# Kernel tuning notes

Hardware: AMD Instinct MI355X
Metric: run time of the kernel (lower is better)

Reference implementation:

```python
import jax, jax.numpy as jnp
import numpy as np

MAX_OOV = 50

def setup_inputs() -> dict:
    key = jax.random.key(0)
    ks = jax.random.split(key, 20)
    B, T, Tc, E, H, V = 128, 256, 200, 256, 512, 50000
    s = 0.02
    inp = {
        'input': jax.random.randint(ks[0], (B, 1), 0, V),
        'h0': jax.random.normal(ks[1], (1, B, H), jnp.float32),
        'c0': jax.random.normal(ks[2], (1, B, H), jnp.float32),
        'encoder_outputs': jax.random.normal(ks[3], (B, T, H), jnp.float32),
        'context_encoder_outputs': jax.random.normal(ks[4], (B, Tc, H), jnp.float32),
        'context_input': jax.random.randint(ks[5], (B, Tc), 0, V + MAX_OOV),
        'embedding': jax.random.normal(ks[6], (V, E), jnp.float32) * s,
        'W_ih': jax.random.normal(ks[7], (4 * H, E), jnp.float32) * s,
        'W_hh': jax.random.normal(ks[8], (4 * H, H), jnp.float32) * s,
        'b_ih': jnp.zeros((4 * H,), jnp.float32),
        'b_hh': jnp.zeros((4 * H,), jnp.float32),
        'attn_W': jax.random.normal(ks[9], (H, H), jnp.float32) * s,
        'attn_b': jnp.zeros((H,), jnp.float32),
        'cattn_W': jax.random.normal(ks[10], (H, H), jnp.float32) * s,
        'cattn_b': jnp.zeros((H,), jnp.float32),
        'gen_W': jax.random.normal(ks[11], (1, 3 * H + E), jnp.float32) * s,
        'gen_b': jnp.zeros((1,), jnp.float32),
        'sig_b': jax.random.uniform(ks[12], (1,), jnp.float32, -0.1, 0.1),
        'out_W': jax.random.normal(ks[13], (V, H), jnp.float32) * s,
        'out_b': jnp.zeros((V,), jnp.float32),
    }
    return inp

def reference(input, h0, c0, encoder_outputs, context_encoder_outputs, context_input,
              embedding, W_ih, W_hh, b_ih, b_hh, attn_W, attn_b, cattn_W, cattn_b,
              gen_W, gen_b, sig_b, out_W, out_b):
    B = input.shape[0]
    V = out_W.shape[0]
    Vext = V + MAX_OOV
    # embedding lookup (input_len == 1)
    emb = embedding[input[:, 0]]                       # [B, E]
    # single-step LSTM (PyTorch gate order: i, f, g, o)
    gates = emb @ W_ih.T + b_ih + h0[0] @ W_hh.T + b_hh  # [B, 4H]
    i, f, g, o = jnp.split(gates, 4, axis=-1)
    c1 = jax.nn.sigmoid(f) * c0[0] + jax.nn.sigmoid(i) * jnp.tanh(g)
    h1 = jax.nn.sigmoid(o) * jnp.tanh(c1)              # [B, H]
    output = h1
    # attention over encoder_outputs (context_only)
    dec = output @ attn_W.T + attn_b                   # [B, H]
    scores = jax.nn.softmax(jnp.einsum('bth,bh->bt', encoder_outputs, dec), axis=1)
    context = jnp.einsum('bt,bth->bh', scores, encoder_outputs)
    # context attention (score_only)
    cdec = output @ cattn_W.T + cattn_b
    cscores = jax.nn.softmax(jnp.einsum('bth,bh->bt', context_encoder_outputs, cdec), axis=1)  # [B, Tc]
    cctx = jnp.einsum('bt,bth->bh', cscores, context_encoder_outputs)
    # generation probability
    feats = jnp.concatenate([context, cctx, output, emb], axis=1)  # [B, 3H+E]
    p_gen = jax.nn.sigmoid(feats @ gen_W.T + gen_b + sig_b)        # [B, 1]
    ctx_len = (context_input > 0).sum(axis=1, keepdims=True)
    p_gen = jnp.where(ctx_len == 0, jnp.float32(1.0), p_gen)
    # vocab distribution, extended with oov zeros
    p_vocab = jax.nn.softmax(output @ out_W.T + out_b, axis=1)
    p_vocab = jnp.concatenate([p_vocab, jnp.zeros((B, MAX_OOV), p_vocab.dtype)], axis=1)
    # copy distribution: scatter-add attention scores into extended vocab
    p_copy = jnp.zeros((B, Vext), p_vocab.dtype).at[
        jnp.arange(B)[:, None], context_input].add(cscores)
    prob = p_gen * p_vocab + (1.0 - p_gen) * p_copy
    logp = jnp.log(jnp.clip(prob, 1e-10))
    return logp, (h1[None], c1[None])
```

## Files before the change

kernel.cpp:

```cpp
#include <hip/hip_runtime.h>
#include <hip/hip_bf16.h>

#define BB 128
#define T_ENC 256
#define T_CTX 200
#define E_DIM 256
#define H_DIM 512
#define V_DIM 50000
#define N_OOV 50
#define VEXT  50050
#define FOURH 2048
#define K_GATES 768
#define LOGP_SZ (BB * VEXT)
#define OUT_H1_OFF LOGP_SZ
#define OUT_C1_OFF (LOGP_SZ + BB * H_DIM)
#define VCHUNK 2048
#define NCHUNK 25

typedef __bf16 bf16x8 __attribute__((ext_vector_type(8)));
typedef float  floatx4 __attribute__((ext_vector_type(4)));

__device__ __forceinline__ float wave_sum(float v) {
#pragma unroll
  for (int m = 32; m > 0; m >>= 1) v += __shfl_xor(v, m, 64);
  return v;
}

__device__ __forceinline__ float sigm(float x) { return 1.0f / (1.0f + __expf(-x)); }

__device__ __forceinline__ unsigned f2bf2(float a, float b) {
  unsigned ua = __float_as_uint(a), ub = __float_as_uint(b);
  ua = (ua + 0x7FFFu + ((ua >> 16) & 1u)) >> 16;
  ub = (ub + 0x7FFFu + ((ub >> 16) & 1u)) & 0xFFFF0000u;
  return ua | ub;
}

__global__ __launch_bounds__(256) void prep_weights(
    const float* __restrict__ W_ih, const float* __restrict__ W_hh,
    const float* __restrict__ attnW, const float* __restrict__ cattnW,
    const float* __restrict__ attnb, const float* __restrict__ cattnb,
    __bf16* __restrict__ Wcat, __bf16* __restrict__ Wattn, float* __restrict__ attnbc) {
  int n = blockIdx.x, tid = threadIdx.x;
  __bf16* wr = Wcat + n * K_GATES;
  wr[tid]       = (__bf16)W_ih[n * E_DIM + tid];
  wr[256 + tid] = (__bf16)W_hh[n * H_DIM + tid];
  wr[512 + tid] = (__bf16)W_hh[n * H_DIM + 256 + tid];
  if (n < 1024) {
    const float* src = (n < 512) ? (attnW + (size_t)n * H_DIM) : (cattnW + (size_t)(n - 512) * H_DIM);
    __bf16* wa = Wattn + n * H_DIM;
    wa[tid]       = (__bf16)src[tid];
    wa[256 + tid] = (__bf16)src[256 + tid];
  }
  if (n < 4) {
    int i = n * 256 + tid;
    attnbc[i] = (i < 512) ? attnb[i] : cattnb[i - 512];
  }
}

__global__ __launch_bounds__(256) void prep_a(
    const int* __restrict__ input, const float* __restrict__ emb_table,
    const float* __restrict__ h0, __bf16* __restrict__ Abuf, float* __restrict__ embf) {
  int b = blockIdx.x, tid = threadIdx.x;
  int tok = input[b];
  float e = emb_table[(size_t)tok * E_DIM + tid];
  embf[b * E_DIM + tid] = e;
  __bf16* ar = Abuf + b * K_GATES;
  ar[tid] = (__bf16)e;
  ar[256 + tid] = (__bf16)h0[b * H_DIM + tid];
  ar[512 + tid] = (__bf16)h0[b * H_DIM + 256 + tid];
}

template <int BF32>
__global__ __launch_bounds__(256) void gemm_mfma(
    const __bf16* __restrict__ Abf, const void* __restrict__ Bsrc,
    const float* __restrict__ bias, float* __restrict__ C, int N, int K, int ldc) {
  __shared__ __bf16 As[128][72];
  __shared__ __bf16 Bs[128][72];
  int tid = threadIdx.x;
  int lane = tid & 63, wid = tid >> 6;
  int wm = wid & 1, wn = wid >> 1;
  int n0 = blockIdx.x * 128;

  floatx4 acc[4][4];
#pragma unroll
  for (int i = 0; i < 4; i++)
#pragma unroll
    for (int j = 0; j < 4; j++) acc[i][j] = (floatx4){0.f, 0.f, 0.f, 0.f};

  int arow = tid >> 1, ahalf = tid & 1;

  for (int k0 = 0; k0 < K; k0 += 64) {
    __syncthreads();
    {
      const uint4* s = (const uint4*)(Abf + arow * K + k0 + ahalf * 32);
      uint4* d = (uint4*)&As[arow][ahalf * 32];
      d[0] = s[0]; d[1] = s[1]; d[2] = s[2]; d[3] = s[3];
    }
    {
      int gn = n0 + arow; if (gn > N - 1) gn = N - 1;
      if (BF32) {
        const float4* s = (const float4*)((const float*)Bsrc + (size_t)gn * K + k0 + ahalf * 32);
        uint4* d = (uint4*)&Bs[arow][ahalf * 32];
#pragma unroll
        for (int q = 0; q < 4; q++) {
          float4 fa = s[2 * q], fb = s[2 * q + 1];
          uint4 o;
          o.x = f2bf2(fa.x, fa.y); o.y = f2bf2(fa.z, fa.w);
          o.z = f2bf2(fb.x, fb.y); o.w = f2bf2(fb.z, fb.w);
          d[q] = o;
        }
      } else {
        const uint4* s = (const uint4*)((const __bf16*)Bsrc + (size_t)gn * K + k0 + ahalf * 32);
        uint4* d = (uint4*)&Bs[arow][ahalf * 32];
        d[0] = s[0]; d[1] = s[1]; d[2] = s[2]; d[3] = s[3];
      }
    }
    __syncthreads();
#pragma unroll
    for (int kk = 0; kk < 64; kk += 32) {
      int kbase = kk + (lane >> 4) * 8;
      bf16x8 a[4], b[4];
#pragma unroll
      for (int i = 0; i < 4; i++) a[i] = *(const bf16x8*)&As[wm * 64 + i * 16 + (lane & 15)][kbase];
#pragma unroll
      for (int j = 0; j < 4; j++) b[j] = *(const bf16x8*)&Bs[wn * 64 + j * 16 + (lane & 15)][kbase];
#pragma unroll
      for (int i = 0; i < 4; i++)
#pragma unroll
        for (int j = 0; j < 4; j++)
          acc[i][j] = __builtin_amdgcn_mfma_f32_16x16x32_bf16(a[i], b[j], acc[i][j], 0, 0, 0);
    }
  }
  int cn = lane & 15, cq = lane >> 4;
#pragma unroll
  for (int i = 0; i < 4; i++)
#pragma unroll
    for (int j = 0; j < 4; j++)
#pragma unroll
      for (int r = 0; r < 4; r++) {
        int row = wm * 64 + i * 16 + cq * 4 + r;
        int col = n0 + wn * 64 + j * 16 + cn;
        if (col < N) {
          float v = acc[i][j][r];
          if (bias) v += bias[col];
          C[(size_t)row * ldc + col] = v;
        }
      }
}

__global__ __launch_bounds__(256) void lstm_kernel(
    const float* __restrict__ gates, const float* __restrict__ b_ih,
    const float* __restrict__ b_hh, const float* __restrict__ c0,
    float* __restrict__ h1_out, float* __restrict__ c1_out, __bf16* __restrict__ h1b) {
  int idx = blockIdx.x * 256 + threadIdx.x;
  int b = idx >> 9, j = idx & 511;
  const float* g = gates + b * FOURH;
  float iv = g[j]        + b_ih[j]        + b_hh[j];
  float fv = g[512 + j]  + b_ih[512 + j]  + b_hh[512 + j];
  float gv = g[1024 + j] + b_ih[1024 + j] + b_hh[1024 + j];
  float ov = g[1536 + j] + b_ih[1536 + j] + b_hh[1536 + j];
  float c1 = sigm(fv) * c0[idx] + sigm(iv) * tanhf(gv);
  float h1 = sigm(ov) * tanhf(c1);
  h1_out[idx] = h1;
  c1_out[idx] = c1;
  h1b[idx] = (__bf16)h1;
}

__global__ __launch_bounds__(256) void flash_attn(
    const float* __restrict__ enc, const float* __restrict__ cenc,
    const float* __restrict__ decbuf, float* __restrict__ opart,
    float2* __restrict__ mlb, float* __restrict__ rawsc) {
  int g = blockIdx.x;
  int b = g & 127;
  int cc = g >> 7;
  int which = cc >> 2, chunk = cc & 3;
  int tchunk = which ? 50 : 64;
  int t0 = chunk * tchunk;
  const float* src = which ? (cenc + (size_t)b * T_CTX * H_DIM) : (enc + (size_t)b * T_ENC * H_DIM);
  const float* decp = decbuf + b * 1024 + which * 512;
  int tid = threadIdx.x, lane = tid & 63, wid = tid >> 6;
  float4 d0 = *(const float4*)(decp + lane * 8);
  float4 d1 = *(const float4*)(decp + lane * 8 + 4);
  float m = -1e30f, l = 0.f;
  float4 o0 = {0.f, 0.f, 0.f, 0.f}, o1 = {0.f, 0.f, 0.f, 0.f};
  for (int t = t0 + wid; t < t0 + tchunk; t += 4) {
    const float* row = src + (size_t)t * H_DIM + lane * 8;
    float4 r0 = *(const float4*)row;
    float4 r1 = *(const float4*)(row + 4);
    float p = r0.x * d0.x + r0.y * d0.y + r0.z * d0.z + r0.w * d0.w +
              r1.x * d1.x + r1.y * d1.y + r1.z * d1.z + r1.w * d1.w;
    p = wave_sum(p);
    if (which && lane == 0) rawsc[b * T_CTX + t] = p;
    float mn = fmaxf(m, p);
    float sc = __expf(m - mn);
    float e  = __expf(p - mn);
    l = l * sc + e;
    o0.x = o0.x * sc + e * r0.x; o0.y = o0.y * sc + e * r0.y;
    o0.z = o0.z * sc + e * r0.z; o0.w = o0.w * sc + e * r0.w;
    o1.x = o1.x * sc + e * r1.x; o1.y = o1.y * sc + e * r1.y;
    o1.z = o1.z * sc + e * r1.z; o1.w = o1.w * sc + e * r1.w;
    m = mn;
  }
  __shared__ float so[4][512];
  __shared__ float sml[4][2];
  *(float4*)&so[wid][lane * 8]     = o0;
  *(float4*)&so[wid][lane * 8 + 4] = o1;
  if (lane == 0) { sml[wid][0] = m; sml[wid][1] = l; }
  __syncthreads();
  float M = fmaxf(fmaxf(sml[0][0], sml[1][0]), fmaxf(sml[2][0], sml[3][0]));
  float w0 = __expf(sml[0][0] - M), w1 = __expf(sml[1][0] - M);
  float w2 = __expf(sml[2][0] - M), w3 = __expf(sml[3][0] - M);
  float L = w0 * sml[0][1] + w1 * sml[1][1] + w2 * sml[2][1] + w3 * sml[3][1];
  int h = tid, h2 = tid + 256;
  float O0 = w0 * so[0][h]  + w1 * so[1][h]  + w2 * so[2][h]  + w3 * so[3][h];
  float O1 = w0 * so[0][h2] + w1 * so[1][h2] + w2 * so[2][h2] + w3 * so[3][h2];
  opart[(size_t)g * 512 + h]  = O0;
  opart[(size_t)g * 512 + h2] = O1;
  if (tid == 0) mlb[g] = make_float2(M, L);
}

__global__ __launch_bounds__(256) void attn_combine(
    const float* __restrict__ opart, const float2* __restrict__ mlb,
    float* __restrict__ ctx, float* __restrict__ cctx,
    float* __restrict__ Mc, float* __restrict__ Lc) {
  int bw = blockIdx.x;
  int b = bw & 127, which = bw >> 7;
  int tid = threadIdx.x;
  int g0 = (which * 4) * 128 + b;
  float2 ml0 = mlb[g0], ml1 = mlb[g0 + 128], ml2 = mlb[g0 + 256], ml3 = mlb[g0 + 384];
  float M = fmaxf(fmaxf(ml0.x, ml1.x), fmaxf(ml2.x, ml3.x));
  float w0 = __expf(ml0.x - M), w1 = __expf(ml1.x - M);
  float w2 = __expf(ml2.x - M), w3 = __expf(ml3.x - M);
  float L = w0 * ml0.y + w1 * ml1.y + w2 * ml2.y + w3 * ml3.y;
  float invL = 1.0f / L;
  float s0 = w0 * opart[(size_t)g0 * 512 + tid]       + w1 * opart[(size_t)(g0 + 128) * 512 + tid] +
             w2 * opart[(size_t)(g0 + 256) * 512 + tid] + w3 * opart[(size_t)(g0 + 384) * 512 + tid];
  int t2 = tid + 256;
  float s1 = w0 * opart[(size_t)g0 * 512 + t2]       + w1 * opart[(size_t)(g0 + 128) * 512 + t2] +
             w2 * opart[(size_t)(g0 + 256) * 512 + t2] + w3 * opart[(size_t)(g0 + 384) * 512 + t2];
  float* outp = (which ? cctx : ctx) + b * 512;
  outp[tid] = s0 * invL;
  outp[t2]  = s1 * invL;
  if (which && tid == 0) { Mc[b] = M; Lc[b] = L; }
}

__global__ __launch_bounds__(256) void pgen_kernel(
    const float* __restrict__ ctx, const float* __restrict__ cctx,
    const float* __restrict__ h1f, const float* __restrict__ embf,
    const float* __restrict__ genW, const float* __restrict__ genb,
    const float* __restrict__ sigb, const int* __restrict__ ctx_inp,
    float* __restrict__ pgen_) {
  int wid = threadIdx.x >> 6, lane = threadIdx.x & 63;
  int b = blockIdx.x * 4 + wid;
  float acc = 0.f;
  for (int j = lane; j < 1792; j += 64) {
    float x;
    if (j < 512) x = ctx[b * 512 + j];
    else if (j < 1024) x = cctx[b * 512 + j - 512];
    else if (j < 1536) x = h1f[b * 512 + j - 1024];
    else x = embf[b * 256 + j - 1536];
    acc += x * genW[j];
  }
  acc = wave_sum(acc);
  float cnt = 0.f;
  for (int j = lane; j < T_CTX; j += 64) cnt += (ctx_inp[b * T_CTX + j] > 0) ? 1.f : 0.f;
  cnt = wave_sum(cnt);
  if (lane == 0) {
    float p = sigm(acc + genb[0] + sigb[0]);
    if (cnt == 0.f) p = 1.0f;
    pgen_[b] = p;
  }
}

__global__ __launch_bounds__(256) void stats_part(
    const float* __restrict__ logits, float* __restrict__ mpart, float* __restrict__ spart) {
  int bx = blockIdx.x;
  int b = bx & 127, c = bx >> 7;
  int tid = threadIdx.x;
  const float* rowp = logits + (size_t)b * VEXT;
  int v0 = c * VCHUNK + tid * 8;
  float m = -1e30f, s = 0.f;
#pragma unroll
  for (int k = 0; k < 4; k++) {
    int v = v0 + 2 * k;
    float2 x = *(const float2*)(rowp + v);
    if (v < V_DIM) {
      float xv = x.x;
      if (xv > m) { s = s * __expf(m - xv) + 1.0f; m = xv; } else s += __expf(xv - m);
    }
    if (v + 1 < V_DIM) {
      float xv = x.y;
      if (xv > m) { s = s * __expf(m - xv) + 1.0f; m = xv; } else s += __expf(xv - m);
    }
  }
  __shared__ float sm[256], ss[256];
  sm[tid] = m; ss[tid] = s; __syncthreads();
  for (int st = 128; st; st >>= 1) {
    if (tid < st) {
      float m2 = sm[tid + st], s2 = ss[tid + st];
      float mo = fmaxf(sm[tid], m2);
      ss[tid] = ss[tid] * __expf(sm[tid] - mo) + s2 * __expf(m2 - mo);
      sm[tid] = mo;
    }
    __syncthreads();
  }
  if (tid == 0) { mpart[bx] = sm[0]; spart[bx] = ss[0]; }
}

__global__ __launch_bounds__(128) void stats_comb(
    const float* __restrict__ mpart, const float* __restrict__ spart,
    float* __restrict__ rowm, float* __restrict__ rows_) {
  int b = threadIdx.x;
  float m = -1e30f, s = 0.f;
#pragma unroll
  for (int c = 0; c < NCHUNK; c++) {
    float m2 = mpart[c * 128 + b], s2 = spart[c * 128 + b];
    float mo = fmaxf(m, m2);
    s = s * __expf(m - mo) + s2 * __expf(m2 - mo);
    m = mo;
  }
  rowm[b] = m; rows_[b] = s;
}

__global__ __launch_bounds__(256) void final_kernel(
    float* __restrict__ out, const int* __restrict__ ctx_inp,
    const float* __restrict__ rawsc, const float* __restrict__ pgen_,
    const float* __restrict__ Mc, const float* __restrict__ Lc,
    const float* __restrict__ rowm, const float* __restrict__ rows_) {
  __shared__ float pc[VCHUNK];
  int bx = blockIdx.x;
  int b = bx & 127, c = bx >> 7;
  int tid = threadIdx.x;
#pragma unroll
  for (int k = 0; k < 8; k++) pc[tid * 8 + k] = 0.f;
  __syncthreads();
  int v0c = c * VCHUNK;
  if (tid < T_CTX) {
    int idx = ctx_inp[b * T_CTX + tid];
    int rel = idx - v0c;
    if (rel >= 0 && rel < VCHUNK) {
      float val = __expf(rawsc[b * T_CTX + tid] - Mc[b]) / Lc[b];
      atomicAdd(&pc[rel], val);
    }
  }
  __syncthreads();
  float pg = pgen_[b], m = rowm[b], inv = 1.0f / rows_[b], pc1 = 1.0f - pg;
  float* rowp = out + (size_t)b * VEXT;
  int li0 = tid * 8;
#pragma unroll
  for (int k = 0; k < 4; k++) {
    int li = li0 + 2 * k;
    int v = v0c + li;
    float2 x = *(const float2*)(rowp + v);
    float pv0 = (v < V_DIM)     ? __expf(x.x - m) * inv : 0.f;
    float pv1 = (v + 1 < V_DIM) ? __expf(x.y - m) * inv : 0.f;
    float r0 = __logf(fmaxf(pg * pv0 + pc1 * pc[li],     1e-10f));
    float r1 = __logf(fmaxf(pg * pv1 + pc1 * pc[li + 1], 1e-10f));
    if (v + 1 < VEXT)      *(float2*)(rowp + v) = make_float2(r0, r1);
    else if (v < VEXT)     rowp[v] = r0;
  }
}

extern "C" void kernel_launch(void* const* d_in, const int* in_sizes, int n_in,
                              void* d_out, int out_size, void* d_ws, size_t ws_size,
                              hipStream_t stream) {
  const int*   input   = (const int*)d_in[0];
  const float* h0      = (const float*)d_in[1];
  const float* c0      = (const float*)d_in[2];
  const float* enc     = (const float*)d_in[3];
  const float* cenc    = (const float*)d_in[4];
  const int*   ctx_inp = (const int*)d_in[5];
  const float* embT    = (const float*)d_in[6];
  const float* W_ih    = (const float*)d_in[7];
  const float* W_hh    = (const float*)d_in[8];
  const float* b_ih    = (const float*)d_in[9];
  const float* b_hh    = (const float*)d_in[10];
  const float* attnW   = (const float*)d_in[11];
  const float* attnb   = (const float*)d_in[12];
  const float* cattnW  = (const float*)d_in[13];
  const float* cattnb  = (const float*)d_in[14];
  const float* genW    = (const float*)d_in[15];
  const float* genb    = (const float*)d_in[16];
  const float* sigb    = (const float*)d_in[17];
  const float* outW    = (const float*)d_in[18];
  const float* outb    = (const float*)d_in[19];

  char* ws = (char*)d_ws;
  __bf16* Wcat   = (__bf16*)(ws + 0);
  __bf16* Wattn  = (__bf16*)(ws + 3145728);
  float*  attnbc = (float*)(ws + 4194304);
  __bf16* Abuf   = (__bf16*)(ws + 4198400);
  float*  embf   = (float*)(ws + 4395008);
  float*  gates  = (float*)(ws + 4526080);
  __bf16* h1b    = (__bf16*)(ws + 5574656);
  float*  decbuf = (float*)(ws + 5705728);
  float*  opart  = (float*)(ws + 6230016);
  float2* mlb    = (float2*)(ws + 8327168);
  float*  ctx    = (float*)(ws + 8335360);
  float*  cctx   = (float*)(ws + 8597504);
  float*  rawsc  = (float*)(ws + 8859648);
  float*  Mc     = (float*)(ws + 8962048);
  float*  Lc     = (float*)(ws + 8962560);
  float*  pgenb  = (float*)(ws + 8963072);
  float*  mpart  = (float*)(ws + 8963584);
  float*  spart  = (float*)(ws + 8976384);
  float*  rowm   = (float*)(ws + 8989184);
  float*  rows_  = (float*)(ws + 8989696);

  float* outF = (float*)d_out;
  float* h1_out = outF + OUT_H1_OFF;
  float* c1_out = outF + OUT_C1_OFF;

  prep_weights<<<2048, 256, 0, stream>>>(W_ih, W_hh, attnW, cattnW, attnb, cattnb, Wcat, Wattn, attnbc);
  prep_a<<<128, 256, 0, stream>>>(input, embT, h0, Abuf, embf);
  gemm_mfma<0><<<16, 256, 0, stream>>>(Abuf, Wcat, nullptr, gates, FOURH, K_GATES, FOURH);
  lstm_kernel<<<256, 256, 0, stream>>>(gates, b_ih, b_hh, c0, h1_out, c1_out, h1b);
  gemm_mfma<1><<<391, 256, 0, stream>>>(h1b, outW, outb, outF, V_DIM, H_DIM, VEXT);
  stats_part<<<NCHUNK * 128, 256, 0, stream>>>(outF, mpart, spart);
  stats_comb<<<1, 128, 0, stream>>>(mpart, spart, rowm, rows_);
  gemm_mfma<0><<<8, 256, 0, stream>>>(h1b, Wattn, attnbc, decbuf, 1024, H_DIM, 1024);
  flash_attn<<<1024, 256, 0, stream>>>(enc, cenc, decbuf, opart, mlb, rawsc);
  attn_combine<<<256, 256, 0, stream>>>(opart, mlb, ctx, cctx, Mc, Lc);
  pgen_kernel<<<32, 256, 0, stream>>>(ctx, cctx, h1_out, embf, genW, genb, sigb, ctx_inp, pgenb);
  final_kernel<<<NCHUNK * 128, 256, 0, stream>>>(outF, ctx_inp, rawsc, pgenb, Mc, Lc, rowm, rows_);
}
```

Measured before the change: 413.0 us.

## Fuse kernels, narrow GEMM tiles to 64 columns, split-K gates GEMM, register prefetch

Cuts the launch count from 12 to 7 by merging the prep kernels, the vocab and attention projection GEMMs, the softmax-stats and flash-attention passes, the two combine steps, and folding the p_gen computation into the final kernel. The GEMM tile shrinks to 128x64 so the vocab projection runs in more blocks (782 instead of 391), and it now prefetches the next K slab into registers while the current one is computed. The gates GEMM is split along K into two halves that the LSTM kernel sums, which adds an extra gates buffer. The final kernel now recomputes p_gen in every one of its 25 chunk blocks per row, which is redundant work.

```diff
diff --git a/kernel.cpp b/kernel.cpp
--- a/kernel.cpp
+++ b/kernel.cpp
@@ -16,6 +16,7 @@
 #define OUT_C1_OFF (LOGP_SZ + BB * H_DIM)
 #define VCHUNK 2048
 #define NCHUNK 25
+#define NBIG 782
 
 typedef __bf16 bf16x8 __attribute__((ext_vector_type(8)));
 typedef float  floatx4 __attribute__((ext_vector_type(4)));
@@ -35,111 +36,128 @@
   return ua | ub;
 }
 
-__global__ __launch_bounds__(256) void prep_weights(
+__global__ __launch_bounds__(256) void prep_all(
     const float* __restrict__ W_ih, const float* __restrict__ W_hh,
     const float* __restrict__ attnW, const float* __restrict__ cattnW,
     const float* __restrict__ attnb, const float* __restrict__ cattnb,
-    __bf16* __restrict__ Wcat, __bf16* __restrict__ Wattn, float* __restrict__ attnbc) {
+    const int* __restrict__ input, const float* __restrict__ embT,
+    const float* __restrict__ h0,
+    __bf16* __restrict__ Wcat, __bf16* __restrict__ Wattn, float* __restrict__ attnbc,
+    __bf16* __restrict__ Abuf, float* __restrict__ embf) {
   int n = blockIdx.x, tid = threadIdx.x;
-  __bf16* wr = Wcat + n * K_GATES;
-  wr[tid]       = (__bf16)W_ih[n * E_DIM + tid];
-  wr[256 + tid] = (__bf16)W_hh[n * H_DIM + tid];
-  wr[512 + tid] = (__bf16)W_hh[n * H_DIM + 256 + tid];
-  if (n < 1024) {
-    const float* src = (n < 512) ? (attnW + (size_t)n * H_DIM) : (cattnW + (size_t)(n - 512) * H_DIM);
-    __bf16* wa = Wattn + n * H_DIM;
-    wa[tid]       = (__bf16)src[tid];
-    wa[256 + tid] = (__bf16)src[256 + tid];
-  }
-  if (n < 4) {
-    int i = n * 256 + tid;
-    attnbc[i] = (i < 512) ? attnb[i] : cattnb[i - 512];
-  }
-}
-
-__global__ __launch_bounds__(256) void prep_a(
-    const int* __restrict__ input, const float* __restrict__ emb_table,
-    const float* __restrict__ h0, __bf16* __restrict__ Abuf, float* __restrict__ embf) {
-  int b = blockIdx.x, tid = threadIdx.x;
-  int tok = input[b];
-  float e = emb_table[(size_t)tok * E_DIM + tid];
-  embf[b * E_DIM + tid] = e;
-  __bf16* ar = Abuf + b * K_GATES;
-  ar[tid] = (__bf16)e;
-  ar[256 + tid] = (__bf16)h0[b * H_DIM + tid];
-  ar[512 + tid] = (__bf16)h0[b * H_DIM + 256 + tid];
+  if (n < 2048) {
+    unsigned* wr = (unsigned*)(Wcat + (size_t)n * K_GATES);
+    for (int idx = tid; idx < 384; idx += 256) {
+      int e0 = idx * 2;
+      float2 x = (e0 < 256) ? *(const float2*)(W_ih + (size_t)n * E_DIM + e0)
+                            : *(const float2*)(W_hh + (size_t)n * H_DIM + e0 - 256);
+      wr[idx] = f2bf2(x.x, x.y);
+    }
+    if (n < 1024) {
+      const float* src = (n < 512) ? (attnW + (size_t)n * H_DIM) : (cattnW + (size_t)(n - 512) * H_DIM);
+      unsigned* wa = (unsigned*)(Wattn + (size_t)n * H_DIM);
+      float2 x = *(const float2*)(src + tid * 2);
+      wa[tid] = f2bf2(x.x, x.y);
+    }
+    if (n < 4) {
+      int i = n * 256 + tid;
+      attnbc[i] = (i < 512) ? attnb[i] : cattnb[i - 512];
+    }
+  } else {
+    int b = n - 2048;
+    int tok = input[b];
+    unsigned* ar = (unsigned*)(Abuf + (size_t)b * K_GATES);
+    for (int idx = tid; idx < 384; idx += 256) {
+      int e0 = idx * 2;
+      float2 x;
+      if (e0 < 256) {
+        x = *(const float2*)(embT + (size_t)tok * E_DIM + e0);
+        *(float2*)(embf + b * E_DIM + e0) = x;
+      } else {
+        x = *(const float2*)(h0 + (size_t)b * H_DIM + e0 - 256);
+      }
+      ar[idx] = f2bf2(x.x, x.y);
+    }
+  }
 }
 
 template <int BF32>
-__global__ __launch_bounds__(256) void gemm_mfma(
+__device__ __forceinline__ void gemm64_body(
     const __bf16* __restrict__ Abf, const void* __restrict__ Bsrc,
-    const float* __restrict__ bias, float* __restrict__ C, int N, int K, int ldc) {
+    const float* __restrict__ bias, float* __restrict__ C,
+    int n0, int N, int Koff, int Klen, int Kpitch, int ldc) {
   __shared__ __bf16 As[128][72];
-  __shared__ __bf16 Bs[128][72];
-  int tid = threadIdx.x;
-  int lane = tid & 63, wid = tid >> 6;
-  int wm = wid & 1, wn = wid >> 1;
-  int n0 = blockIdx.x * 128;
-
-  floatx4 acc[4][4];
-#pragma unroll
-  for (int i = 0; i < 4; i++)
+  __shared__ __bf16 Bs[64][72];
+  int tid = threadIdx.x, lane = tid & 63, wid = tid >> 6;
+
+  floatx4 acc[2][4];
+#pragma unroll
+  for (int i = 0; i < 2; i++)
 #pragma unroll
     for (int j = 0; j < 4; j++) acc[i][j] = (floatx4){0.f, 0.f, 0.f, 0.f};
 
   int arow = tid >> 1, ahalf = tid & 1;
-
-  for (int k0 = 0; k0 < K; k0 += 64) {
+  int brow = tid >> 2, bq = tid & 3;
+  int gnb = n0 + brow; if (gnb > N - 1) gnb = N - 1;
+
+  const __bf16* abase = Abf + (size_t)arow * Kpitch + Koff + ahalf * 32;
+  const float*  bfb = (const float*)Bsrc + (size_t)gnb * Kpitch + Koff + bq * 16;
+  const __bf16* bhb = (const __bf16*)Bsrc + (size_t)gnb * Kpitch + Koff + bq * 16;
+
+  uint4 ra[4];
+  float4 rbf[4];
+  uint4 rbh[2];
+  {
+    const uint4* s = (const uint4*)abase;
+    ra[0] = s[0]; ra[1] = s[1]; ra[2] = s[2]; ra[3] = s[3];
+    if (BF32) { const float4* t = (const float4*)bfb; rbf[0] = t[0]; rbf[1] = t[1]; rbf[2] = t[2]; rbf[3] = t[3]; }
+    else      { const uint4* t = (const uint4*)bhb;  rbh[0] = t[0]; rbh[1] = t[1]; }
+  }
+
+  for (int k0 = 0; k0 < Klen; k0 += 64) {
     __syncthreads();
-    {
-      const uint4* s = (const uint4*)(Abf + arow * K + k0 + ahalf * 32);
-      uint4* d = (uint4*)&As[arow][ahalf * 32];
-      d[0] = s[0]; d[1] = s[1]; d[2] = s[2]; d[3] = s[3];
-    }
-    {
-      int gn = n0 + arow; if (gn > N - 1) gn = N - 1;
-      if (BF32) {
-        const float4* s = (const float4*)((const float*)Bsrc + (size_t)gn * K + k0 + ahalf * 32);
-        uint4* d = (uint4*)&Bs[arow][ahalf * 32];
-#pragma unroll
-        for (int q = 0; q < 4; q++) {
-          float4 fa = s[2 * q], fb = s[2 * q + 1];
-          uint4 o;
-          o.x = f2bf2(fa.x, fa.y); o.y = f2bf2(fa.z, fa.w);
-          o.z = f2bf2(fb.x, fb.y); o.w = f2bf2(fb.z, fb.w);
-          d[q] = o;
-        }
-      } else {
-        const uint4* s = (const uint4*)((const __bf16*)Bsrc + (size_t)gn * K + k0 + ahalf * 32);
-        uint4* d = (uint4*)&Bs[arow][ahalf * 32];
-        d[0] = s[0]; d[1] = s[1]; d[2] = s[2]; d[3] = s[3];
-      }
+    { uint4* d = (uint4*)&As[arow][ahalf * 32]; d[0] = ra[0]; d[1] = ra[1]; d[2] = ra[2]; d[3] = ra[3]; }
+    if (BF32) {
+      uint4 o0, o1;
+      o0.x = f2bf2(rbf[0].x, rbf[0].y); o0.y = f2bf2(rbf[0].z, rbf[0].w);
+      o0.z = f2bf2(rbf[1].x, rbf[1].y); o0.w = f2bf2(rbf[1].z, rbf[1].w);
+      o1.x = f2bf2(rbf[2].x, rbf[2].y); o1.y = f2bf2(rbf[2].z, rbf[2].w);
+      o1.z = f2bf2(rbf[3].x, rbf[3].y); o1.w = f2bf2(rbf[3].z, rbf[3].w);
+      uint4* d = (uint4*)&Bs[brow][bq * 16]; d[0] = o0; d[1] = o1;
+    } else {
+      uint4* d = (uint4*)&Bs[brow][bq * 16]; d[0] = rbh[0]; d[1] = rbh[1];
+    }
+    if (k0 + 64 < Klen) {
+      const uint4* s = (const uint4*)(abase + k0 + 64);
+      ra[0] = s[0]; ra[1] = s[1]; ra[2] = s[2]; ra[3] = s[3];
+      if (BF32) { const float4* t = (const float4*)(bfb + k0 + 64); rbf[0] = t[0]; rbf[1] = t[1]; rbf[2] = t[2]; rbf[3] = t[3]; }
+      else      { const uint4* t = (const uint4*)(bhb + k0 + 64);  rbh[0] = t[0]; rbh[1] = t[1]; }
     }
     __syncthreads();
 #pragma unroll
     for (int kk = 0; kk < 64; kk += 32) {
       int kbase = kk + (lane >> 4) * 8;
-      bf16x8 a[4], b[4];
-#pragma unroll
-      for (int i = 0; i < 4; i++) a[i] = *(const bf16x8*)&As[wm * 64 + i * 16 + (lane & 15)][kbase];
-#pragma unroll
-      for (int j = 0; j < 4; j++) b[j] = *(const bf16x8*)&Bs[wn * 64 + j * 16 + (lane & 15)][kbase];
-#pragma unroll
-      for (int i = 0; i < 4; i++)
-#pragma unroll
-        for (int j = 0; j < 4; j++)
-          acc[i][j] = __builtin_amdgcn_mfma_f32_16x16x32_bf16(a[i], b[j], acc[i][j], 0, 0, 0);
+      bf16x8 a0 = *(const bf16x8*)&As[wid * 32 + (lane & 15)][kbase];
+      bf16x8 a1 = *(const bf16x8*)&As[wid * 32 + 16 + (lane & 15)][kbase];
+      bf16x8 bfr[4];
+#pragma unroll
+      for (int j = 0; j < 4; j++) bfr[j] = *(const bf16x8*)&Bs[j * 16 + (lane & 15)][kbase];
+#pragma unroll
+      for (int j = 0; j < 4; j++) {
+        acc[0][j] = __builtin_amdgcn_mfma_f32_16x16x32_bf16(a0, bfr[j], acc[0][j], 0, 0, 0);
+        acc[1][j] = __builtin_amdgcn_mfma_f32_16x16x32_bf16(a1, bfr[j], acc[1][j], 0, 0, 0);
+      }
     }
   }
   int cn = lane & 15, cq = lane >> 4;
 #pragma unroll
-  for (int i = 0; i < 4; i++)
+  for (int i = 0; i < 2; i++)
 #pragma unroll
     for (int j = 0; j < 4; j++)
 #pragma unroll
       for (int r = 0; r < 4; r++) {
-        int row = wm * 64 + i * 16 + cq * 4 + r;
-        int col = n0 + wn * 64 + j * 16 + cn;
+        int row = wid * 32 + i * 16 + cq * 4 + r;
+        int col = n0 + j * 16 + cn;
         if (col < N) {
           float v = acc[i][j][r];
           if (bias) v += bias[col];
@@ -148,17 +166,37 @@
       }
 }
 
+__global__ __launch_bounds__(256) void gates_gemm(
+    const __bf16* __restrict__ Abuf, const __bf16* __restrict__ Wcat,
+    float* __restrict__ g0, float* __restrict__ g1) {
+  int bx = blockIdx.x;
+  int kh = bx >> 5, nb = bx & 31;
+  gemm64_body<0>(Abuf, Wcat, nullptr, kh ? g1 : g0, nb * 64, FOURH, kh * 384, 384, K_GATES, FOURH);
+}
+
+__global__ __launch_bounds__(256) void mega_gemm(
+    const __bf16* __restrict__ h1b, const float* __restrict__ outW,
+    const float* __restrict__ outb, float* __restrict__ Cbig,
+    const __bf16* __restrict__ Wattn, const float* __restrict__ attnbc,
+    float* __restrict__ decbuf) {
+  int bx = blockIdx.x;
+  if (bx < NBIG) gemm64_body<1>(h1b, outW, outb, Cbig, bx * 64, V_DIM, 0, H_DIM, H_DIM, VEXT);
+  else           gemm64_body<0>(h1b, Wattn, attnbc, decbuf, (bx - NBIG) * 64, 1024, 0, H_DIM, H_DIM, 1024);
+}
+
 __global__ __launch_bounds__(256) void lstm_kernel(
-    const float* __restrict__ gates, const float* __restrict__ b_ih,
-    const float* __restrict__ b_hh, const float* __restrict__ c0,
+    const float* __restrict__ gA, const float* __restrict__ gB,
+    const float* __restrict__ b_ih, const float* __restrict__ b_hh,
+    const float* __restrict__ c0,
     float* __restrict__ h1_out, float* __restrict__ c1_out, __bf16* __restrict__ h1b) {
   int idx = blockIdx.x * 256 + threadIdx.x;
   int b = idx >> 9, j = idx & 511;
-  const float* g = gates + b * FOURH;
-  float iv = g[j]        + b_ih[j]        + b_hh[j];
-  float fv = g[512 + j]  + b_ih[512 + j]  + b_hh[512 + j];
-  float gv = g[1024 + j] + b_ih[1024 + j] + b_hh[1024 + j];
-  float ov = g[1536 + j] + b_ih[1536 + j] + b_hh[1536 + j];
+  const float* ga = gA + b * FOURH;
+  const float* gb = gB + b * FOURH;
+  float iv = ga[j]        + gb[j]        + b_ih[j]        + b_hh[j];
+  float fv = ga[512 + j]  + gb[512 + j]  + b_ih[512 + j]  + b_hh[512 + j];
+  float gv = ga[1024 + j] + gb[1024 + j] + b_ih[1024 + j] + b_hh[1024 + j];
+  float ov = ga[1536 + j] + gb[1536 + j] + b_ih[1536 + j] + b_hh[1536 + j];
   float c1 = sigm(fv) * c0[idx] + sigm(iv) * tanhf(gv);
   float h1 = sigm(ov) * tanhf(c1);
   h1_out[idx] = h1;
@@ -166,11 +204,12 @@
   h1b[idx] = (__bf16)h1;
 }
 
-__global__ __launch_bounds__(256) void flash_attn(
-    const float* __restrict__ enc, const float* __restrict__ cenc,
+__device__ __forceinline__ void flash_body(
+    int g, const float* __restrict__ enc, const float* __restrict__ cenc,
     const float* __restrict__ decbuf, float* __restrict__ opart,
     float2* __restrict__ mlb, float* __restrict__ rawsc) {
-  int g = blockIdx.x;
+  __shared__ float so[4][512];
+  __shared__ float sml[4][2];
   int b = g & 127;
   int cc = g >> 7;
   int which = cc >> 2, chunk = cc & 3;
@@ -201,8 +240,6 @@
     o1.z = o1.z * sc + e * r1.z; o1.w = o1.w * sc + e * r1.w;
     m = mn;
   }
-  __shared__ float so[4][512];
-  __shared__ float sml[4][2];
   *(float4*)&so[wid][lane * 8]     = o0;
   *(float4*)&so[wid][lane * 8 + 4] = o1;
   if (lane == 0) { sml[wid][0] = m; sml[wid][1] = l; }
@@ -219,62 +256,10 @@
   if (tid == 0) mlb[g] = make_float2(M, L);
 }
 
-__global__ __launch_bounds__(256) void attn_combine(
-    const float* __restrict__ opart, const float2* __restrict__ mlb,
-    float* __restrict__ ctx, float* __restrict__ cctx,
-    float* __restrict__ Mc, float* __restrict__ Lc) {
-  int bw = blockIdx.x;
-  int b = bw & 127, which = bw >> 7;
-  int tid = threadIdx.x;
-  int g0 = (which * 4) * 128 + b;
-  float2 ml0 = mlb[g0], ml1 = mlb[g0 + 128], ml2 = mlb[g0 + 256], ml3 = mlb[g0 + 384];
-  float M = fmaxf(fmaxf(ml0.x, ml1.x), fmaxf(ml2.x, ml3.x));
-  float w0 = __expf(ml0.x - M), w1 = __expf(ml1.x - M);
-  float w2 = __expf(ml2.x - M), w3 = __expf(ml3.x - M);
-  float L = w0 * ml0.y + w1 * ml1.y + w2 * ml2.y + w3 * ml3.y;
-  float invL = 1.0f / L;
-  float s0 = w0 * opart[(size_t)g0 * 512 + tid]       + w1 * opart[(size_t)(g0 + 128) * 512 + tid] +
-             w2 * opart[(size_t)(g0 + 256) * 512 + tid] + w3 * opart[(size_t)(g0 + 384) * 512 + tid];
-  int t2 = tid + 256;
-  float s1 = w0 * opart[(size_t)g0 * 512 + t2]       + w1 * opart[(size_t)(g0 + 128) * 512 + t2] +
-             w2 * opart[(size_t)(g0 + 256) * 512 + t2] + w3 * opart[(size_t)(g0 + 384) * 512 + t2];
-  float* outp = (which ? cctx : ctx) + b * 512;
-  outp[tid] = s0 * invL;
-  outp[t2]  = s1 * invL;
-  if (which && tid == 0) { Mc[b] = M; Lc[b] = L; }
-}
-
-__global__ __launch_bounds__(256) void pgen_kernel(
-    const float* __restrict__ ctx, const float* __restrict__ cctx,
-    const float* __restrict__ h1f, const float* __restrict__ embf,
-    const float* __restrict__ genW, const float* __restrict__ genb,
-    const float* __restrict__ sigb, const int* __restrict__ ctx_inp,
-    float* __restrict__ pgen_) {
-  int wid = threadIdx.x >> 6, lane = threadIdx.x & 63;
-  int b = blockIdx.x * 4 + wid;
-  float acc = 0.f;
-  for (int j = lane; j < 1792; j += 64) {
-    float x;
-    if (j < 512) x = ctx[b * 512 + j];
-    else if (j < 1024) x = cctx[b * 512 + j - 512];
-    else if (j < 1536) x = h1f[b * 512 + j - 1024];
-    else x = embf[b * 256 + j - 1536];
-    acc += x * genW[j];
-  }
-  acc = wave_sum(acc);
-  float cnt = 0.f;
-  for (int j = lane; j < T_CTX; j += 64) cnt += (ctx_inp[b * T_CTX + j] > 0) ? 1.f : 0.f;
-  cnt = wave_sum(cnt);
-  if (lane == 0) {
-    float p = sigm(acc + genb[0] + sigb[0]);
-    if (cnt == 0.f) p = 1.0f;
-    pgen_[b] = p;
-  }
-}
-
-__global__ __launch_bounds__(256) void stats_part(
-    const float* __restrict__ logits, float* __restrict__ mpart, float* __restrict__ spart) {
-  int bx = blockIdx.x;
+__device__ __forceinline__ void stats_body(
+    int bx, const float* __restrict__ logits,
+    float* __restrict__ mpart, float* __restrict__ spart) {
+  __shared__ float sm[256], ss[256];
   int b = bx & 127, c = bx >> 7;
   int tid = threadIdx.x;
   const float* rowp = logits + (size_t)b * VEXT;
@@ -293,7 +278,6 @@
       if (xv > m) { s = s * __expf(m - xv) + 1.0f; m = xv; } else s += __expf(xv - m);
     }
   }
-  __shared__ float sm[256], ss[256];
   sm[tid] = m; ss[tid] = s; __syncthreads();
   for (int st = 128; st; st >>= 1) {
     if (tid < st) {
@@ -307,44 +291,102 @@
   if (tid == 0) { mpart[bx] = sm[0]; spart[bx] = ss[0]; }
 }
 
-__global__ __launch_bounds__(128) void stats_comb(
+__global__ __launch_bounds__(256) void fs_kernel(
+    const float* __restrict__ logits, float* __restrict__ mpart, float* __restrict__ spart,
+    const float* __restrict__ enc, const float* __restrict__ cenc,
+    const float* __restrict__ decbuf, float* __restrict__ opart,
+    float2* __restrict__ mlb, float* __restrict__ rawsc) {
+  int bx = blockIdx.x;
+  if (bx < NCHUNK * 128) stats_body(bx, logits, mpart, spart);
+  else flash_body(bx - NCHUNK * 128, enc, cenc, decbuf, opart, mlb, rawsc);
+}
+
+__global__ __launch_bounds__(256) void comb_kernel(
+    const float* __restrict__ opart, const float2* __restrict__ mlb,
+    float* __restrict__ ctx, float* __restrict__ cctx,
+    float* __restrict__ Mc, float* __restrict__ Lc,
     const float* __restrict__ mpart, const float* __restrict__ spart,
     float* __restrict__ rowm, float* __restrict__ rows_) {
-  int b = threadIdx.x;
-  float m = -1e30f, s = 0.f;
-#pragma unroll
-  for (int c = 0; c < NCHUNK; c++) {
-    float m2 = mpart[c * 128 + b], s2 = spart[c * 128 + b];
-    float mo = fmaxf(m, m2);
-    s = s * __expf(m - mo) + s2 * __expf(m2 - mo);
-    m = mo;
-  }
-  rowm[b] = m; rows_[b] = s;
+  int bw = blockIdx.x;
+  int tid = threadIdx.x;
+  if (bw < 256) {
+    int b = bw & 127, which = bw >> 7;
+    int g0 = (which * 4) * 128 + b;
+    float2 ml0 = mlb[g0], ml1 = mlb[g0 + 128], ml2 = mlb[g0 + 256], ml3 = mlb[g0 + 384];
+    float M = fmaxf(fmaxf(ml0.x, ml1.x), fmaxf(ml2.x, ml3.x));
+    float w0 = __expf(ml0.x - M), w1 = __expf(ml1.x - M);
+    float w2 = __expf(ml2.x - M), w3 = __expf(ml3.x - M);
+    float L = w0 * ml0.y + w1 * ml1.y + w2 * ml2.y + w3 * ml3.y;
+    float invL = 1.0f / L;
+    float s0 = w0 * opart[(size_t)g0 * 512 + tid]         + w1 * opart[(size_t)(g0 + 128) * 512 + tid] +
+               w2 * opart[(size_t)(g0 + 256) * 512 + tid] + w3 * opart[(size_t)(g0 + 384) * 512 + tid];
+    int t2 = tid + 256;
+    float s1 = w0 * opart[(size_t)g0 * 512 + t2]          + w1 * opart[(size_t)(g0 + 128) * 512 + t2] +
+               w2 * opart[(size_t)(g0 + 256) * 512 + t2]  + w3 * opart[(size_t)(g0 + 384) * 512 + t2];
+    float* outp = (which ? cctx : ctx) + b * 512;
+    outp[tid] = s0 * invL;
+    outp[t2]  = s1 * invL;
+    if (which && tid == 0) { Mc[b] = M; Lc[b] = L; }
+  } else if (tid < 128) {
+    int b = tid;
+    float m = -1e30f, s = 0.f;
+#pragma unroll
+    for (int c = 0; c < NCHUNK; c++) {
+      float m2 = mpart[c * 128 + b], s2 = spart[c * 128 + b];
+      float mo = fmaxf(m, m2);
+      s = s * __expf(m - mo) + s2 * __expf(m2 - mo);
+      m = mo;
+    }
+    rowm[b] = m; rows_[b] = s;
+  }
 }
 
 __global__ __launch_bounds__(256) void final_kernel(
     float* __restrict__ out, const int* __restrict__ ctx_inp,
-    const float* __restrict__ rawsc, const float* __restrict__ pgen_,
-    const float* __restrict__ Mc, const float* __restrict__ Lc,
-    const float* __restrict__ rowm, const float* __restrict__ rows_) {
+    const float* __restrict__ rawsc, const float* __restrict__ Mc, const float* __restrict__ Lc,
+    const float* __restrict__ rowm, const float* __restrict__ rows_,
+    const float* __restrict__ ctx, const float* __restrict__ cctx,
+    const float* __restrict__ h1f, const float* __restrict__ embf,
+    const float* __restrict__ genW, const float* __restrict__ genb,
+    const float* __restrict__ sigb) {
   __shared__ float pc[VCHUNK];
+  __shared__ float red8[8];
   int bx = blockIdx.x;
   int b = bx & 127, c = bx >> 7;
-  int tid = threadIdx.x;
+  int tid = threadIdx.x, lane = tid & 63, wid = tid >> 6;
+  int cidx = (tid < T_CTX) ? ctx_inp[b * T_CTX + tid] : 0;
+  float acc = 0.f;
+  for (int j = tid; j < 1792; j += 256) {
+    float x;
+    if (j < 512) x = ctx[b * 512 + j];
+    else if (j < 1024) x = cctx[b * 512 + j - 512];
+    else if (j < 1536) x = h1f[b * 512 + j - 1024];
+    else x = embf[b * 256 + j - 1536];
+    acc += x * genW[j];
+  }
+  float cnt = (tid < T_CTX && cidx > 0) ? 1.f : 0.f;
+  acc = wave_sum(acc); cnt = wave_sum(cnt);
+  if (lane == 0) { red8[wid] = acc; red8[4 + wid] = cnt; }
 #pragma unroll
   for (int k = 0; k < 8; k++) pc[tid * 8 + k] = 0.f;
   __syncthreads();
+  float pg;
+  {
+    float a = red8[0] + red8[1] + red8[2] + red8[3];
+    float cn = red8[4] + red8[5] + red8[6] + red8[7];
+    pg = sigm(a + genb[0] + sigb[0]);
+    if (cn == 0.f) pg = 1.0f;
+  }
   int v0c = c * VCHUNK;
   if (tid < T_CTX) {
-    int idx = ctx_inp[b * T_CTX + tid];
-    int rel = idx - v0c;
+    int rel = cidx - v0c;
     if (rel >= 0 && rel < VCHUNK) {
       float val = __expf(rawsc[b * T_CTX + tid] - Mc[b]) / Lc[b];
       atomicAdd(&pc[rel], val);
     }
   }
   __syncthreads();
-  float pg = pgen_[b], m = rowm[b], inv = 1.0f / rows_[b], pc1 = 1.0f - pg;
+  float m = rowm[b], inv = 1.0f / rows_[b], pc1 = 1.0f - pg;
   float* rowp = out + (size_t)b * VEXT;
   int li0 = tid * 8;
 #pragma unroll
@@ -392,35 +434,33 @@
   __bf16* Abuf   = (__bf16*)(ws + 4198400);
   float*  embf   = (float*)(ws + 4395008);
   float*  gates  = (float*)(ws + 4526080);
-  __bf16* h1b    = (__bf16*)(ws + 5574656);
-  float*  decbuf = (float*)(ws + 5705728);
-  float*  opart  = (float*)(ws + 6230016);
-  float2* mlb    = (float2*)(ws + 8327168);
-  float*  ctx    = (float*)(ws + 8335360);
-  float*  cctx   = (float*)(ws + 8597504);
-  float*  rawsc  = (float*)(ws + 8859648);
-  float*  Mc     = (float*)(ws + 8962048);
-  float*  Lc     = (float*)(ws + 8962560);
-  float*  pgenb  = (float*)(ws + 8963072);
-  float*  mpart  = (float*)(ws + 8963584);
-  float*  spart  = (float*)(ws + 8976384);
-  float*  rowm   = (float*)(ws + 8989184);
-  float*  rows_  = (float*)(ws + 8989696);
+  float*  gates2 = (float*)(ws + 5574656);
+  __bf16* h1b    = (__bf16*)(ws + 6623232);
+  float*  decbuf = (float*)(ws + 6754304);
+  float*  opart  = (float*)(ws + 7278592);
+  float2* mlb    = (float2*)(ws + 9375744);
+  float*  ctx    = (float*)(ws + 9383936);
+  float*  cctx   = (float*)(ws + 9646080);
+  float*  rawsc  = (float*)(ws + 9908224);
+  float*  Mc     = (float*)(ws + 10010624);
+  float*  Lc     = (float*)(ws + 10011136);
+  float*  mpart  = (float*)(ws + 10011648);
+  float*  spart  = (float*)(ws + 10024448);
+  float*  rowm   = (float*)(ws + 10037248);
+  float*  rows_  = (float*)(ws + 10037760);
 
   float* outF = (float*)d_out;
   float* h1_out = outF + OUT_H1_OFF;
   float* c1_out = outF + OUT_C1_OFF;
 
-  prep_weights<<<2048, 256, 0, stream>>>(W_ih, W_hh, attnW, cattnW, attnb, cattnb, Wcat, Wattn, attnbc);
-  prep_a<<<128, 256, 0, stream>>>(input, embT, h0, Abuf, embf);
-  gemm_mfma<0><<<16, 256, 0, stream>>>(Abuf, Wcat, nullptr, gates, FOURH, K_GATES, FOURH);
-  lstm_kernel<<<256, 256, 0, stream>>>(gates, b_ih, b_hh, c0, h1_out, c1_out, h1b);
-  gemm_mfma<1><<<391, 256, 0, stream>>>(h1b, outW, outb, outF, V_DIM, H_DIM, VEXT);
-  stats_part<<<NCHUNK * 128, 256, 0, stream>>>(outF, mpart, spart);
-  stats_comb<<<1, 128, 0, stream>>>(mpart, spart, rowm, rows_);
-  gemm_mfma<0><<<8, 256, 0, stream>>>(h1b, Wattn, attnbc, decbuf, 1024, H_DIM, 1024);
-  flash_attn<<<1024, 256, 0, stream>>>(enc, cenc, decbuf, opart, mlb, rawsc);
-  attn_combine<<<256, 256, 0, stream>>>(opart, mlb, ctx, cctx, Mc, Lc);
-  pgen_kernel<<<32, 256, 0, stream>>>(ctx, cctx, h1_out, embf, genW, genb, sigb, ctx_inp, pgenb);
-  final_kernel<<<NCHUNK * 128, 256, 0, stream>>>(outF, ctx_inp, rawsc, pgenb, Mc, Lc, rowm, rows_);
-}
+  prep_all<<<2176, 256, 0, stream>>>(W_ih, W_hh, attnW, cattnW, attnb, cattnb,
+                                     input, embT, h0, Wcat, Wattn, attnbc, Abuf, embf);
+  gates_gemm<<<64, 256, 0, stream>>>(Abuf, Wcat, gates, gates2);
+  lstm_kernel<<<256, 256, 0, stream>>>(gates, gates2, b_ih, b_hh, c0, h1_out, c1_out, h1b);
+  mega_gemm<<<NBIG + 16, 256, 0, stream>>>(h1b, outW, outb, outF, Wattn, attnbc, decbuf);
+  fs_kernel<<<NCHUNK * 128 + 1024, 256, 0, stream>>>(outF, mpart, spart,
+                                                     enc, cenc, decbuf, opart, mlb, rawsc);
+  comb_kernel<<<257, 256, 0, stream>>>(opart, mlb, ctx, cctx, Mc, Lc, mpart, spart, rowm, rows_);
+  final_kernel<<<NCHUNK * 128, 256, 0, stream>>>(outF, ctx_inp, rawsc, Mc, Lc, rowm, rows_,
+                                                 ctx, cctx, h1_out, embf, genW, genb, sigb);
+}
```

Measured after the change: 392.5 us. -5.0%, faster.
